# Optimization experiments

Measured on AMD Instinct MI355X. Metric: run time of the kernel, lower is better.

Reference implementation:

```python
import jax, jax.numpy as jnp
import numpy as np

# --- dims derived from init_kwargs ---
K = 16                 # top-k patches
NUM_SAMPLES = 500      # MC samples for perturbed top-k
SIGMA = 0.05
PATCH = 128            # patch_size
H_SCORE, W_SCORE = 16, 16
SCALE_H, SCALE_W = 64, 64          # high // score
# padding per DPS.__init__: padded = scale*score + patch - 1
TOP_PAD = (PATCH - SCALE_H) // 2    # 32
LEFT_PAD = (PATCH - SCALE_W) // 2   # 32
BOTTOM_PAD = (SCALE_H * H_SCORE + PATCH - 1) - TOP_PAD - 1024   # 95
RIGHT_PAD = (SCALE_W * W_SCORE + PATCH - 1) - LEFT_PAD - 1024   # 95


def setup_inputs() -> dict:
    key = jax.random.key(0)
    k1, k2 = jax.random.split(key)
    x_high = jax.random.normal(k1, (8, 3, 1024, 1024), dtype=jnp.float32)
    scores_2d = jax.random.uniform(k2, (8, H_SCORE, W_SCORE), dtype=jnp.float32)
    return {"x_high": x_high, "scores_2d": scores_2d}


def _perturbed_topk_indicators(scores):
    # scores: (b, d) ; faithful to PerturbedTopKFunction.forward
    b, d = scores.shape
    noise = jax.random.normal(jax.random.key(42), (b, NUM_SAMPLES, d), dtype=scores.dtype)
    perturbed = scores[:, None, :] + noise * SIGMA          # (b, n, d)
    idx = jax.lax.top_k(perturbed, K)[1]                    # (b, n, k)
    idx = jnp.sort(idx, axis=-1)                            # torch sorts indices ascending
    onehot = jax.nn.one_hot(idx, d, dtype=scores.dtype)     # (b, n, k, d)
    return onehot.mean(axis=1)                              # (b, k, d)


def _dps_forward(x_high, scores_2d, indicators_fn):
    b, c = x_high.shape[:2]
    # min-max normalize scores
    s = scores_2d.reshape(b, -1)
    smin = s.min(axis=-1, keepdims=True)
    smax = s.max(axis=-1, keepdims=True)
    s = (s - smin) / (smax - smin + 1e-5)
    ind = indicators_fn(s).reshape(b, K, H_SCORE, W_SCORE)  # soft top-k indicators

    x_pad = jnp.pad(x_high, ((0, 0), (0, 0), (TOP_PAD, BOTTOM_PAD), (LEFT_PAD, RIGHT_PAD)))
    # column window indices for all w_score grid cells: (W_SCORE, PATCH)
    col_idx = (jnp.arange(W_SCORE) * SCALE_W)[:, None] + jnp.arange(PATCH)[None, :]

    def row_step(acc, i):
        # rows of all patches in grid-row i: (b, c, PATCH, W_pad)
        row = jax.lax.dynamic_slice_in_dim(x_pad, i * SCALE_H, PATCH, axis=2)
        wins = row[:, :, :, col_idx]                        # (b, c, PATCH, W_SCORE, PATCH)
        w = jax.lax.dynamic_slice_in_dim(ind, i, 1, axis=2)[:, :, 0, :]  # (b, k, W_SCORE)
        acc = acc + jnp.einsum('bcpwq,bkw->bkcpq', wins, w)
        return acc, None

    patches0 = jnp.zeros((b, K, c, PATCH, PATCH), dtype=x_high.dtype)
    patches, _ = jax.lax.scan(row_step, patches0, jnp.arange(H_SCORE))
    return patches.reshape(-1, c, PATCH, PATCH)


def reference(x_high, scores_2d):
    return _dps_forward(x_high, scores_2d, _perturbed_topk_indicators)
```

## Files before the change

### kernel.cpp

```cpp
#include <hip/hip_runtime.h>
#include <stdint.h>


#define NSAMP 500
#define DDIM  256

__device__ __forceinline__ void threefry2x32_0_42(uint32_t x0, uint32_t x1,
                                                  uint32_t& o0, uint32_t& o1) {
  const uint32_t k0 = 0u, k1 = 42u;
  const uint32_t k2 = k0 ^ k1 ^ 0x1BD11BDAu;
  x0 += k0; x1 += k1;
#define TF_ROUND(r) { x0 += x1; x1 = (x1 << (r)) | (x1 >> (32 - (r))); x1 ^= x0; }
  TF_ROUND(13) TF_ROUND(15) TF_ROUND(26) TF_ROUND(6)
  x0 += k1; x1 += k2 + 1u;
  TF_ROUND(17) TF_ROUND(29) TF_ROUND(16) TF_ROUND(24)
  x0 += k2; x1 += k0 + 2u;
  TF_ROUND(13) TF_ROUND(15) TF_ROUND(26) TF_ROUND(6)
  x0 += k0; x1 += k1 + 3u;
  TF_ROUND(17) TF_ROUND(29) TF_ROUND(16) TF_ROUND(24)
  x0 += k1; x1 += k2 + 4u;
  TF_ROUND(13) TF_ROUND(15) TF_ROUND(26) TF_ROUND(6)
  x0 += k2; x1 += k0 + 5u;
#undef TF_ROUND
  o0 = x0; o1 = x1;
}

__device__ __forceinline__ float xla_erfinv(float x) {
#pragma clang fp contract(off)
  float w = -log1pf(-x * x);
  float p;
  if (w < 5.0f) {
    w = w - 2.5f;
    p = 2.81022636e-08f;
    p = 3.43273939e-07f + p * w;
    p = -3.5233877e-06f + p * w;
    p = -4.39150654e-06f + p * w;
    p = 0.00021858087f + p * w;
    p = -0.00125372503f + p * w;
    p = -0.00417768164f + p * w;
    p = 0.246640727f + p * w;
    p = 1.50140941f + p * w;
  } else {
    w = sqrtf(w) - 3.0f;
    p = -0.000200214257f;
    p = 0.000100950558f + p * w;
    p = 0.00134934322f + p * w;
    p = -0.00367342844f + p * w;
    p = 0.00573950773f + p * w;
    p = -0.0076224613f + p * w;
    p = 0.00943887047f + p * w;
    p = 1.00167406f + p * w;
    p = 2.83297682f + p * w;
  }
  return p * x;
}

__global__ void __launch_bounds__(256) topk_kernel(const float* __restrict__ scores,
                                                   uint32_t* __restrict__ counts) {
#pragma clang fp contract(off)
  const int gs = blockIdx.x;
  const int b = gs / NSAMP;
  const int n = gs - b * NSAMP;
  const int d = threadIdx.x;
  const int lane = d & 63, wv = d >> 6;

  __shared__ float wmx[4], wmn[4];
  __shared__ float wtl[4];
  __shared__ int   wcc[4];
  __shared__ __align__(16) float candPv[DDIM];
  __shared__ int   candIdx[DDIM];
  __shared__ unsigned char selMark[DDIM];
  __shared__ int wtot[4];

  const float sc = scores[b * DDIM + d];

  float mx = sc, mn = sc;
  for (int off = 32; off > 0; off >>= 1) {
    mx = fmaxf(mx, __shfl_xor(mx, off));
    mn = fminf(mn, __shfl_xor(mn, off));
  }
  if (lane == 0) { wmx[wv] = mx; wmn[wv] = mn; }
  selMark[d] = 0;
  __syncthreads();
  mx = fmaxf(fmaxf(wmx[0], wmx[1]), fmaxf(wmx[2], wmx[3]));
  mn = fminf(fminf(wmn[0], wmn[1]), fminf(wmn[2], wmn[3]));
  const float denom = (mx - mn) + 1e-5f;

  const uint32_t j = (uint32_t)(b * (NSAMP * DDIM) + n * DDIM + d);
  uint32_t o0, o1;
  threefry2x32_0_42(0u, j, o0, o1);
  const uint32_t bits = o0 ^ o1;
  const float flo = -0.99999994f;
  float f = __uint_as_float((bits >> 9) | 0x3f800000u) - 1.0f;
  float u = f * 2.0f + flo;
  u = fmaxf(flo, u);
  const float z = 1.41421356237f * xla_erfinv(u);
  const float sv = (sc - mn) / denom;
  const float pv = sv + z * 0.05f;

  float gmx = pv;
  gmx = fmaxf(gmx, __shfl_xor(gmx, 1));
  gmx = fmaxf(gmx, __shfl_xor(gmx, 2));
  gmx = fmaxf(gmx, __shfl_xor(gmx, 4));
  gmx = fmaxf(gmx, __shfl_xor(gmx, 8));
  float tl = gmx;
  tl = fminf(tl, __shfl_xor(tl, 16));
  tl = fminf(tl, __shfl_xor(tl, 32));
  if (lane == 0) wtl[wv] = tl;
  __syncthreads();
  const float T_lb = fminf(fminf(wtl[0], wtl[1]), fminf(wtl[2], wtl[3]));

  const bool cand = (pv >= T_lb);
  const unsigned long long cm = __ballot(cand);
  if (lane == 0) wcc[wv] = __popcll(cm);
  __syncthreads();
  int cbase = 0;
  for (int w2 = 0; w2 < wv; ++w2) cbase += wcc[w2];
  const int C = wcc[0] + wcc[1] + wcc[2] + wcc[3];
  if (cand) {
    const int pos = cbase + __popcll(cm & ((1ull << lane) - 1ull));
    candPv[pos] = pv;
    candIdx[pos] = d;
  }
  const int Cr = (C + 3) & ~3;
  if (d >= C && d < Cr) candPv[d] = -1e30f;
  __syncthreads();

  if (d < C) {
    const float cpv = candPv[d];
    int gc = 0, eqb = 0;
    const float4* c4 = (const float4*)candPv;
    for (int e4 = 0; e4 < (Cr >> 2); ++e4) {
      const float4 o = c4[e4];
      const int e = e4 << 2;
      gc += (o.x > cpv); gc += (o.y > cpv); gc += (o.z > cpv); gc += (o.w > cpv);
      eqb += (o.x == cpv) & ((e + 0) < d);
      eqb += (o.y == cpv) & ((e + 1) < d);
      eqb += (o.z == cpv) & ((e + 2) < d);
      eqb += (o.w == cpv) & ((e + 3) < d);
    }
    if ((gc + eqb) < 16) selMark[candIdx[d]] = 1;
  }
  __syncthreads();

  const bool sel = selMark[d] != 0;
  const unsigned long long m = __ballot(sel);
  if (lane == 0) wtot[wv] = __popcll(m);
  __syncthreads();
  int r = __popcll(m & ((1ull << lane) - 1ull));
  for (int w2 = 0; w2 < wv; ++w2) r += wtot[w2];

  if (sel) atomicAdd(&counts[(b << 12) + (r << 8) + d], 1u);
}

__global__ void __launch_bounds__(256) patches_kernel(const float* __restrict__ x,
                                                      const uint32_t* __restrict__ counts,
                                                      float* __restrict__ out) {
  const int p0 = blockIdx.x << 3;
  const int c  = blockIdx.y;
  const int zb = blockIdx.z;
  const int b  = zb >> 1;
  const int k0 = (zb & 1) << 3;

  __shared__ __align__(16) float cw[DDIM * 8];
  __shared__ int colOff[DDIM];
  __shared__ int wcnt[4];

  const int tid = threadIdx.x;
  const int lane = tid & 63, wvi = tid >> 6;

  {
    float wreg[8];
    bool any = false;
#pragma unroll
    for (int kk = 0; kk < 8; ++kk) {
      float w = (float)counts[((b * 16 + k0 + kk) << 8) + tid] / 500.0f;
      wreg[kk] = w;
      any = any || (w != 0.0f);
    }
    unsigned long long m = __ballot(any);
    if (lane == 0) wcnt[wvi] = __popcll(m);
    __syncthreads();
    int base = 0;
    for (int w2 = 0; w2 < wvi; ++w2) base += wcnt[w2];
    if (any) {
      int pos = base + __popcll(m & ((1ull << lane) - 1ull));
      colOff[pos] = ((tid >> 4) << 16) | ((tid & 15) << 6);
#pragma unroll
      for (int kk = 0; kk < 8; ++kk) cw[pos * 8 + kk] = wreg[kk];
    }
    __syncthreads();
  }
  const int nact = wcnt[0] + wcnt[1] + wcnt[2] + wcnt[3];

  const int q0   = (tid & 31) << 2;
  const int slot = tid >> 5;
  const int ps   = p0 + slot;

  int qm = 0xFFFF, ym = 0xFFFF;
  if (q0 < 32) qm &= ~1;
  if (q0 > 92) qm &= ~0x8000;
  if (ps < 32) ym &= ~1;
  if (ps > 95) ym &= ~0x8000;
  const int baseOff = (ps - 32) * 1024 + q0 - 32;

  float4 acc[8];
#pragma unroll
  for (int kk = 0; kk < 8; ++kk) acc[kk] = make_float4(0.f, 0.f, 0.f, 0.f);

  const float* xim = x + ((size_t)(b * 3 + c) << 20);

  float4 xv = make_float4(0.f, 0.f, 0.f, 0.f);
  int okc = 0;
  if (nact > 0) {
    const int co = colOff[0];
    okc = (qm >> ((co >> 6) & 15)) & (ym >> (co >> 16)) & 1;
    xv = *(const float4*)(xim + (okc ? (baseOff + co) : 0));
  }

  for (int it = 0; it < nact; ++it) {
    const int itn = (it + 1 < nact) ? it + 1 : it;
    const int con = colOff[itn];
    const int okn = (qm >> ((con >> 6) & 15)) & (ym >> (con >> 16)) & 1;
    const float4 xn = *(const float4*)(xim + (okn ? (baseOff + con) : 0));

    float4 xc = xv;
    xc.x = okc ? xc.x : 0.0f;
    xc.y = okc ? xc.y : 0.0f;
    xc.z = okc ? xc.z : 0.0f;
    xc.w = okc ? xc.w : 0.0f;

    const float4 wa = *(const float4*)&cw[it * 8 + 0];
    const float4 wb = *(const float4*)&cw[it * 8 + 4];

#define ACC_K(kk, wv_)                                            \
    { acc[kk].x += (wv_) * xc.x; acc[kk].y += (wv_) * xc.y;       \
      acc[kk].z += (wv_) * xc.z; acc[kk].w += (wv_) * xc.w; }
    ACC_K(0, wa.x) ACC_K(1, wa.y) ACC_K(2, wa.z) ACC_K(3, wa.w)
    ACC_K(4, wb.x) ACC_K(5, wb.y) ACC_K(6, wb.z) ACC_K(7, wb.w)
#undef ACC_K

    xv = xn;
    okc = okn;
  }

#pragma unroll
  for (int kk = 0; kk < 8; ++kk) {
    const size_t obase = ((size_t)((b * 16 + k0 + kk) * 3 + c)) << 14;
    float4* dst = (float4*)(out + obase + (size_t)ps * 128 + q0);
    __builtin_nontemporal_store(acc[kk].x, &dst->x);
    __builtin_nontemporal_store(acc[kk].y, &dst->y);
    __builtin_nontemporal_store(acc[kk].z, &dst->z);
    __builtin_nontemporal_store(acc[kk].w, &dst->w);
  }
}

extern "C" void kernel_launch(void* const* d_in, const int* in_sizes, int n_in,
                              void* d_out, int out_size, void* d_ws, size_t ws_size,
                              hipStream_t stream) {
  const float* x_high = (const float*)d_in[0];
  const float* scores = (const float*)d_in[1];
  float* out = (float*)d_out;
  uint32_t* counts = (uint32_t*)d_ws;

  hipMemsetAsync(counts, 0, 8 * 16 * DDIM * sizeof(uint32_t), stream);
  topk_kernel<<<8 * NSAMP, 256, 0, stream>>>(scores, counts);
  patches_kernel<<<dim3(16, 3, 16), 256, 0, stream>>>(x_high, counts, out);
}
```

Measured before the change: 171.6 us.

## Fuse top-k and patch kernels into one persistent kernel with grid barrier and L2 prefetch

```diff
diff --git a/kernel.cpp b/kernel.cpp
--- a/kernel.cpp
+++ b/kernel.cpp
@@ -4,6 +4,7 @@
 
 #define NSAMP 500
 #define DDIM  256
+#define GRID  512
 
 __device__ __forceinline__ void threefry2x32_0_42(uint32_t x0, uint32_t x1,
                                                   uint32_t& o0, uint32_t& o1) {
@@ -55,203 +56,224 @@
   return p * x;
 }
 
-__global__ void __launch_bounds__(256) topk_kernel(const float* __restrict__ scores,
-                                                   uint32_t* __restrict__ counts) {
+__global__ void __launch_bounds__(256, 2)
+fused_kernel(const float* __restrict__ x, const float* __restrict__ scores,
+             uint32_t* __restrict__ counts, uint32_t* __restrict__ bar,
+             float* __restrict__ out) {
+  const int lb  = blockIdx.x;
+  const int tid = threadIdx.x;
+  const int lane = tid & 63, wv = tid >> 6;
+
+  __shared__ float s_wmx[4], s_wmn[4], s_wtl[4];
+  __shared__ int   s_wcc[4], s_wtot[4];
+  __shared__ __align__(16) float s_candPv[DDIM];
+  __shared__ int   s_candIdx[DDIM];
+  __shared__ unsigned char s_selMark[DDIM];
+  __shared__ __align__(16) float s_cw[DDIM * 8];
+  __shared__ int s_colOff[DDIM];
+  __shared__ int s_wcnt[4];
+
+  {
 #pragma clang fp contract(off)
-  const int gs = blockIdx.x;
-  const int b = gs / NSAMP;
-  const int n = gs - b * NSAMP;
-  const int d = threadIdx.x;
-  const int lane = d & 63, wv = d >> 6;
-
-  __shared__ float wmx[4], wmn[4];
-  __shared__ float wtl[4];
-  __shared__ int   wcc[4];
-  __shared__ __align__(16) float candPv[DDIM];
-  __shared__ int   candIdx[DDIM];
-  __shared__ unsigned char selMark[DDIM];
-  __shared__ int wtot[4];
-
-  const float sc = scores[b * DDIM + d];
-
-  float mx = sc, mn = sc;
-  for (int off = 32; off > 0; off >>= 1) {
-    mx = fmaxf(mx, __shfl_xor(mx, off));
-    mn = fminf(mn, __shfl_xor(mn, off));
-  }
-  if (lane == 0) { wmx[wv] = mx; wmn[wv] = mn; }
-  selMark[d] = 0;
+    const int d = tid;
+    for (int gs = lb; gs < 8 * NSAMP; gs += GRID) {
+      const float4* pfp = (const float4*)x + (size_t)gs * 1572;
+      const float4 pf0 = pfp[(tid << 1) + 0];
+      const float4 pf1 = pfp[(tid << 1) + 1];
+
+      const int b = gs / NSAMP;
+      const int n = gs - b * NSAMP;
+
+      const float sc = scores[b * DDIM + d];
+
+      float mx = sc, mn = sc;
+      for (int off = 32; off > 0; off >>= 1) {
+        mx = fmaxf(mx, __shfl_xor(mx, off));
+        mn = fminf(mn, __shfl_xor(mn, off));
+      }
+      if (lane == 0) { s_wmx[wv] = mx; s_wmn[wv] = mn; }
+      s_selMark[d] = 0;
+      __syncthreads();
+      mx = fmaxf(fmaxf(s_wmx[0], s_wmx[1]), fmaxf(s_wmx[2], s_wmx[3]));
+      mn = fminf(fminf(s_wmn[0], s_wmn[1]), fminf(s_wmn[2], s_wmn[3]));
+      const float denom = (mx - mn) + 1e-5f;
+
+      const uint32_t j = (uint32_t)(b * (NSAMP * DDIM) + n * DDIM + d);
+      uint32_t o0, o1;
+      threefry2x32_0_42(0u, j, o0, o1);
+      const uint32_t bits = o0 ^ o1;
+      const float flo = -0.99999994f;
+      float f = __uint_as_float((bits >> 9) | 0x3f800000u) - 1.0f;
+      float u = f * 2.0f + flo;
+      u = fmaxf(flo, u);
+      const float z = 1.41421356237f * xla_erfinv(u);
+      const float sv = (sc - mn) / denom;
+      const float pv = sv + z * 0.05f;
+
+      float gmx = pv;
+      gmx = fmaxf(gmx, __shfl_xor(gmx, 1));
+      gmx = fmaxf(gmx, __shfl_xor(gmx, 2));
+      gmx = fmaxf(gmx, __shfl_xor(gmx, 4));
+      gmx = fmaxf(gmx, __shfl_xor(gmx, 8));
+      float tl = gmx;
+      tl = fminf(tl, __shfl_xor(tl, 16));
+      tl = fminf(tl, __shfl_xor(tl, 32));
+      if (lane == 0) s_wtl[wv] = tl;
+      __syncthreads();
+      const float T_lb = fminf(fminf(s_wtl[0], s_wtl[1]), fminf(s_wtl[2], s_wtl[3]));
+
+      const bool candf = (pv >= T_lb);
+      const unsigned long long cm = __ballot(candf);
+      if (lane == 0) s_wcc[wv] = __popcll(cm);
+      __syncthreads();
+      int cbase = 0;
+      for (int w2 = 0; w2 < wv; ++w2) cbase += s_wcc[w2];
+      const int C = s_wcc[0] + s_wcc[1] + s_wcc[2] + s_wcc[3];
+      if (candf) {
+        const int pos = cbase + __popcll(cm & ((1ull << lane) - 1ull));
+        s_candPv[pos] = pv;
+        s_candIdx[pos] = d;
+      }
+      const int Cr = (C + 3) & ~3;
+      if (d >= C && d < Cr) s_candPv[d] = -1e30f;
+      __syncthreads();
+
+      if (d < C) {
+        const float cpv = s_candPv[d];
+        int gc = 0, eqb = 0;
+        const float4* c4 = (const float4*)s_candPv;
+        for (int e4 = 0; e4 < (Cr >> 2); ++e4) {
+          const float4 o = c4[e4];
+          const int e = e4 << 2;
+          gc += (o.x > cpv); gc += (o.y > cpv); gc += (o.z > cpv); gc += (o.w > cpv);
+          eqb += (o.x == cpv) & ((e + 0) < d);
+          eqb += (o.y == cpv) & ((e + 1) < d);
+          eqb += (o.z == cpv) & ((e + 2) < d);
+          eqb += (o.w == cpv) & ((e + 3) < d);
+        }
+        if ((gc + eqb) < 16) s_selMark[s_candIdx[d]] = 1;
+      }
+      __syncthreads();
+
+      const bool sel = s_selMark[d] != 0;
+      const unsigned long long m = __ballot(sel);
+      if (lane == 0) s_wtot[wv] = __popcll(m);
+      __syncthreads();
+      int r = __popcll(m & ((1ull << lane) - 1ull));
+      for (int w2 = 0; w2 < wv; ++w2) r += s_wtot[w2];
+
+      if (sel) atomicAdd(&counts[(b << 12) + (r << 8) + d], 1u);
+
+      asm volatile("" :: "v"(pf0.x), "v"(pf0.y), "v"(pf0.z), "v"(pf0.w),
+                         "v"(pf1.x), "v"(pf1.y), "v"(pf1.z), "v"(pf1.w));
+      __syncthreads();
+    }
+  }
+
+  __threadfence();
   __syncthreads();
-  mx = fmaxf(fmaxf(wmx[0], wmx[1]), fmaxf(wmx[2], wmx[3]));
-  mn = fminf(fminf(wmn[0], wmn[1]), fminf(wmn[2], wmn[3]));
-  const float denom = (mx - mn) + 1e-5f;
-
-  const uint32_t j = (uint32_t)(b * (NSAMP * DDIM) + n * DDIM + d);
-  uint32_t o0, o1;
-  threefry2x32_0_42(0u, j, o0, o1);
-  const uint32_t bits = o0 ^ o1;
-  const float flo = -0.99999994f;
-  float f = __uint_as_float((bits >> 9) | 0x3f800000u) - 1.0f;
-  float u = f * 2.0f + flo;
-  u = fmaxf(flo, u);
-  const float z = 1.41421356237f * xla_erfinv(u);
-  const float sv = (sc - mn) / denom;
-  const float pv = sv + z * 0.05f;
-
-  float gmx = pv;
-  gmx = fmaxf(gmx, __shfl_xor(gmx, 1));
-  gmx = fmaxf(gmx, __shfl_xor(gmx, 2));
-  gmx = fmaxf(gmx, __shfl_xor(gmx, 4));
-  gmx = fmaxf(gmx, __shfl_xor(gmx, 8));
-  float tl = gmx;
-  tl = fminf(tl, __shfl_xor(tl, 16));
-  tl = fminf(tl, __shfl_xor(tl, 32));
-  if (lane == 0) wtl[wv] = tl;
+  if (tid == 0) {
+    __hip_atomic_fetch_add(bar, 1u, __ATOMIC_ACQ_REL, __HIP_MEMORY_SCOPE_AGENT);
+    while (__hip_atomic_load(bar, __ATOMIC_ACQUIRE, __HIP_MEMORY_SCOPE_AGENT)
+           < gridDim.x) {
+      __builtin_amdgcn_s_sleep(2);
+    }
+  }
   __syncthreads();
-  const float T_lb = fminf(fminf(wtl[0], wtl[1]), fminf(wtl[2], wtl[3]));
-
-  const bool cand = (pv >= T_lb);
-  const unsigned long long cm = __ballot(cand);
-  if (lane == 0) wcc[wv] = __popcll(cm);
-  __syncthreads();
-  int cbase = 0;
-  for (int w2 = 0; w2 < wv; ++w2) cbase += wcc[w2];
-  const int C = wcc[0] + wcc[1] + wcc[2] + wcc[3];
-  if (cand) {
-    const int pos = cbase + __popcll(cm & ((1ull << lane) - 1ull));
-    candPv[pos] = pv;
-    candIdx[pos] = d;
-  }
-  const int Cr = (C + 3) & ~3;
-  if (d >= C && d < Cr) candPv[d] = -1e30f;
-  __syncthreads();
-
-  if (d < C) {
-    const float cpv = candPv[d];
-    int gc = 0, eqb = 0;
-    const float4* c4 = (const float4*)candPv;
-    for (int e4 = 0; e4 < (Cr >> 2); ++e4) {
-      const float4 o = c4[e4];
-      const int e = e4 << 2;
-      gc += (o.x > cpv); gc += (o.y > cpv); gc += (o.z > cpv); gc += (o.w > cpv);
-      eqb += (o.x == cpv) & ((e + 0) < d);
-      eqb += (o.y == cpv) & ((e + 1) < d);
-      eqb += (o.z == cpv) & ((e + 2) < d);
-      eqb += (o.w == cpv) & ((e + 3) < d);
-    }
-    if ((gc + eqb) < 16) selMark[candIdx[d]] = 1;
-  }
-  __syncthreads();
-
-  const bool sel = selMark[d] != 0;
-  const unsigned long long m = __ballot(sel);
-  if (lane == 0) wtot[wv] = __popcll(m);
-  __syncthreads();
-  int r = __popcll(m & ((1ull << lane) - 1ull));
-  for (int w2 = 0; w2 < wv; ++w2) r += wtot[w2];
-
-  if (sel) atomicAdd(&counts[(b << 12) + (r << 8) + d], 1u);
-}
-
-__global__ void __launch_bounds__(256) patches_kernel(const float* __restrict__ x,
-                                                      const uint32_t* __restrict__ counts,
-                                                      float* __restrict__ out) {
-  const int p0 = blockIdx.x << 3;
-  const int c  = blockIdx.y;
-  const int zb = blockIdx.z;
-  const int b  = zb >> 1;
-  const int k0 = (zb & 1) << 3;
-
-  __shared__ __align__(16) float cw[DDIM * 8];
-  __shared__ int colOff[DDIM];
-  __shared__ int wcnt[4];
-
-  const int tid = threadIdx.x;
-  const int lane = tid & 63, wvi = tid >> 6;
-
-  {
-    float wreg[8];
-    bool any = false;
+  __threadfence();
+
+  for (int uu = lb; uu < 768; uu += GRID) {
+    __syncthreads();
+    const int p0 = (uu & 15) << 3;
+    const int c  = (uu >> 4) % 3;
+    const int zb = uu / 48;
+    const int b  = zb >> 1;
+    const int k0 = (zb & 1) << 3;
+
+    {
+      float wreg[8];
+      bool any = false;
+#pragma unroll
+      for (int kk = 0; kk < 8; ++kk) {
+        float w = (float)counts[((b * 16 + k0 + kk) << 8) + tid] / 500.0f;
+        wreg[kk] = w;
+        any = any || (w != 0.0f);
+      }
+      unsigned long long m = __ballot(any);
+      if (lane == 0) s_wcnt[wv] = __popcll(m);
+      __syncthreads();
+      int base = 0;
+      for (int w2 = 0; w2 < wv; ++w2) base += s_wcnt[w2];
+      if (any) {
+        int pos = base + __popcll(m & ((1ull << lane) - 1ull));
+        s_colOff[pos] = ((tid >> 4) << 16) | ((tid & 15) << 6);
+#pragma unroll
+        for (int kk = 0; kk < 8; ++kk) s_cw[pos * 8 + kk] = wreg[kk];
+      }
+      __syncthreads();
+    }
+    const int nact = s_wcnt[0] + s_wcnt[1] + s_wcnt[2] + s_wcnt[3];
+
+    const int q0   = (tid & 31) << 2;
+    const int slot = tid >> 5;
+    const int ps   = p0 + slot;
+
+    int qm = 0xFFFF, ym = 0xFFFF;
+    if (q0 < 32) qm &= ~1;
+    if (q0 > 92) qm &= ~0x8000;
+    if (ps < 32) ym &= ~1;
+    if (ps > 95) ym &= ~0x8000;
+    const int baseOff = (ps - 32) * 1024 + q0 - 32;
+
+    float4 acc[8];
+#pragma unroll
+    for (int kk = 0; kk < 8; ++kk) acc[kk] = make_float4(0.f, 0.f, 0.f, 0.f);
+
+    const float* xim = x + ((size_t)(b * 3 + c) << 20);
+
+    float4 xv = make_float4(0.f, 0.f, 0.f, 0.f);
+    int okc = 0;
+    if (nact > 0) {
+      const int co = s_colOff[0];
+      okc = (qm >> ((co >> 6) & 15)) & (ym >> (co >> 16)) & 1;
+      xv = *(const float4*)(xim + (okc ? (baseOff + co) : 0));
+    }
+
+    for (int it = 0; it < nact; ++it) {
+      const int itn = (it + 1 < nact) ? it + 1 : it;
+      const int con = s_colOff[itn];
+      const int okn = (qm >> ((con >> 6) & 15)) & (ym >> (con >> 16)) & 1;
+      const float4 xn = *(const float4*)(xim + (okn ? (baseOff + con) : 0));
+
+      float4 xc = xv;
+      xc.x = okc ? xc.x : 0.0f;
+      xc.y = okc ? xc.y : 0.0f;
+      xc.z = okc ? xc.z : 0.0f;
+      xc.w = okc ? xc.w : 0.0f;
+
+      const float4 wa = *(const float4*)&s_cw[it * 8 + 0];
+      const float4 wb = *(const float4*)&s_cw[it * 8 + 4];
+
+#define ACC_K(kk, wv_)                                            \
+      { acc[kk].x += (wv_) * xc.x; acc[kk].y += (wv_) * xc.y;     \
+        acc[kk].z += (wv_) * xc.z; acc[kk].w += (wv_) * xc.w; }
+      ACC_K(0, wa.x) ACC_K(1, wa.y) ACC_K(2, wa.z) ACC_K(3, wa.w)
+      ACC_K(4, wb.x) ACC_K(5, wb.y) ACC_K(6, wb.z) ACC_K(7, wb.w)
+#undef ACC_K
+
+      xv = xn;
+      okc = okn;
+    }
+
 #pragma unroll
     for (int kk = 0; kk < 8; ++kk) {
-      float w = (float)counts[((b * 16 + k0 + kk) << 8) + tid] / 500.0f;
-      wreg[kk] = w;
-      any = any || (w != 0.0f);
-    }
-    unsigned long long m = __ballot(any);
-    if (lane == 0) wcnt[wvi] = __popcll(m);
-    __syncthreads();
-    int base = 0;
-    for (int w2 = 0; w2 < wvi; ++w2) base += wcnt[w2];
-    if (any) {
-      int pos = base + __popcll(m & ((1ull << lane) - 1ull));
-      colOff[pos] = ((tid >> 4) << 16) | ((tid & 15) << 6);
-#pragma unroll
-      for (int kk = 0; kk < 8; ++kk) cw[pos * 8 + kk] = wreg[kk];
-    }
-    __syncthreads();
-  }
-  const int nact = wcnt[0] + wcnt[1] + wcnt[2] + wcnt[3];
-
-  const int q0   = (tid & 31) << 2;
-  const int slot = tid >> 5;
-  const int ps   = p0 + slot;
-
-  int qm = 0xFFFF, ym = 0xFFFF;
-  if (q0 < 32) qm &= ~1;
-  if (q0 > 92) qm &= ~0x8000;
-  if (ps < 32) ym &= ~1;
-  if (ps > 95) ym &= ~0x8000;
-  const int baseOff = (ps - 32) * 1024 + q0 - 32;
-
-  float4 acc[8];
-#pragma unroll
-  for (int kk = 0; kk < 8; ++kk) acc[kk] = make_float4(0.f, 0.f, 0.f, 0.f);
-
-  const float* xim = x + ((size_t)(b * 3 + c) << 20);
-
-  float4 xv = make_float4(0.f, 0.f, 0.f, 0.f);
-  int okc = 0;
-  if (nact > 0) {
-    const int co = colOff[0];
-    okc = (qm >> ((co >> 6) & 15)) & (ym >> (co >> 16)) & 1;
-    xv = *(const float4*)(xim + (okc ? (baseOff + co) : 0));
-  }
-
-  for (int it = 0; it < nact; ++it) {
-    const int itn = (it + 1 < nact) ? it + 1 : it;
-    const int con = colOff[itn];
-    const int okn = (qm >> ((con >> 6) & 15)) & (ym >> (con >> 16)) & 1;
-    const float4 xn = *(const float4*)(xim + (okn ? (baseOff + con) : 0));
-
-    float4 xc = xv;
-    xc.x = okc ? xc.x : 0.0f;
-    xc.y = okc ? xc.y : 0.0f;
-    xc.z = okc ? xc.z : 0.0f;
-    xc.w = okc ? xc.w : 0.0f;
-
-    const float4 wa = *(const float4*)&cw[it * 8 + 0];
-    const float4 wb = *(const float4*)&cw[it * 8 + 4];
-
-#define ACC_K(kk, wv_)                                            \
-    { acc[kk].x += (wv_) * xc.x; acc[kk].y += (wv_) * xc.y;       \
-      acc[kk].z += (wv_) * xc.z; acc[kk].w += (wv_) * xc.w; }
-    ACC_K(0, wa.x) ACC_K(1, wa.y) ACC_K(2, wa.z) ACC_K(3, wa.w)
-    ACC_K(4, wb.x) ACC_K(5, wb.y) ACC_K(6, wb.z) ACC_K(7, wb.w)
-#undef ACC_K
-
-    xv = xn;
-    okc = okn;
-  }
-
-#pragma unroll
-  for (int kk = 0; kk < 8; ++kk) {
-    const size_t obase = ((size_t)((b * 16 + k0 + kk) * 3 + c)) << 14;
-    float4* dst = (float4*)(out + obase + (size_t)ps * 128 + q0);
-    __builtin_nontemporal_store(acc[kk].x, &dst->x);
-    __builtin_nontemporal_store(acc[kk].y, &dst->y);
-    __builtin_nontemporal_store(acc[kk].z, &dst->z);
-    __builtin_nontemporal_store(acc[kk].w, &dst->w);
+      const size_t obase = ((size_t)((b * 16 + k0 + kk) * 3 + c)) << 14;
+      float4* dst = (float4*)(out + obase + (size_t)ps * 128 + q0);
+      __builtin_nontemporal_store(acc[kk].x, &dst->x);
+      __builtin_nontemporal_store(acc[kk].y, &dst->y);
+      __builtin_nontemporal_store(acc[kk].z, &dst->z);
+      __builtin_nontemporal_store(acc[kk].w, &dst->w);
+    }
   }
 }
 
@@ -262,8 +284,8 @@
   const float* scores = (const float*)d_in[1];
   float* out = (float*)d_out;
   uint32_t* counts = (uint32_t*)d_ws;
-
-  hipMemsetAsync(counts, 0, 8 * 16 * DDIM * sizeof(uint32_t), stream);
-  topk_kernel<<<8 * NSAMP, 256, 0, stream>>>(scores, counts);
-  patches_kernel<<<dim3(16, 3, 16), 256, 0, stream>>>(x_high, counts, out);
-}
+  uint32_t* bar = counts + 8 * 16 * DDIM;
+
+  hipMemsetAsync(counts, 0, (8 * 16 * DDIM + 16) * sizeof(uint32_t), stream);
+  fused_kernel<<<GRID, 256, 0, stream>>>(x_high, scores, counts, bar, out);
+}
```

Result: slower. 305.5 us (+78.0%).
